# Performance work log

Hardware: AMD Instinct MI355X
Metric: run time of the kernel (lower is better)

## Reference

```python
import jax, jax.numpy as jnp
import numpy as np

H = 4        # num_heads
KNN = 10     # k_knn neighbors gathered by distance
KS = 4       # k_select top-k neighbors kept by attention score
EPS = 1e-5
BIG = 1e9


def _ln(x, g, b):
    m = x.mean(-1, keepdims=True)
    v = ((x - m) ** 2).mean(-1, keepdims=True)
    return (x - m) * jax.lax.rsqrt(v + EPS) * g + b


def _sparse_dyn_voxel_attn(x, coords, mask, w_qkv, b_qkv, w_proj, b_proj):
    # x: [B,N,C], coords: [B,N,3], mask: [B,N] bool
    B, N, C = x.shape
    dh = C // H
    qkv = x @ w_qkv + b_qkv                       # [B,N,3C]
    q, k, v = jnp.split(qkv, 3, axis=-1)
    q = q.reshape(B, N, H, dh).transpose(0, 2, 1, 3)   # [B,H,N,dh]
    k = k.reshape(B, N, H, dh).transpose(0, 2, 1, 3)
    v = v.reshape(B, N, H, dh).transpose(0, 2, 1, 3)

    # KNN over voxel coordinates; empty voxels pushed to far distance
    d2 = jnp.sum((coords[:, :, None, :] - coords[:, None, :, :]) ** 2, axis=-1)  # [B,N,N]
    d2 = jnp.where(mask[:, None, :], d2, BIG)
    _, nbr = jax.lax.top_k(-d2, KNN)              # [B,N,KNN] nearest-neighbor indices

    # gather neighbor keys/values: [B,H,N,KNN,dh]
    kn = jax.vmap(lambda a, i: a[:, i, :])(k, nbr)
    vn = jax.vmap(lambda a, i: a[:, i, :])(v, nbr)
    nmask = jax.vmap(lambda m, i: m[i])(mask, nbr)  # [B,N,KNN]

    scale = float(1.0 / np.sqrt(dh))
    scores = jnp.einsum('bhnd,bhnkd->bhnk', q, kn) * scale  # [B,H,N,KNN]
    scores = scores + jnp.where(nmask, 0.0, -BIG)[:, None, :, :]

    # dynamic selection: keep top k_select neighbors by score, softmax over them
    sv, si = jax.lax.top_k(scores, KS)            # [B,H,N,KS]
    w = jax.nn.softmax(sv, axis=-1)
    vsel = jnp.take_along_axis(vn, si[..., None], axis=3)   # [B,H,N,KS,dh]
    o = jnp.einsum('bhnk,bhnkd->bhnd', w, vsel)   # [B,H,N,dh]
    o = o.transpose(0, 2, 1, 3).reshape(B, N, C) @ w_proj + b_proj
    return jnp.where(mask[..., None], o, 0.0)


def setup_inputs() -> dict:
    key = jax.random.key(0)
    ks = jax.random.split(key, 8)
    B, N, C, M = 4, 4096, 64, 256  # N = 16^3 voxels
    s = lambda k, sh: jax.random.normal(k, sh, jnp.float32) * 0.02
    return dict(
        inputs=jax.random.normal(ks[0], (B, N, C), jnp.float32),
        voxel_coords=jax.random.uniform(ks[1], (B, N, 3), jnp.float32) * 16.0,
        non_empty_mask=jax.random.randint(ks[2], (B, N), 0, 2).astype(bool),
        ln1_g=jnp.ones(C, jnp.float32), ln1_b=jnp.zeros(C, jnp.float32),
        ln2_g=jnp.ones(C, jnp.float32), ln2_b=jnp.zeros(C, jnp.float32),
        w_qkv=s(ks[3], (C, 3 * C)), b_qkv=jnp.zeros(3 * C, jnp.float32),
        w_proj=s(ks[4], (C, C)), b_proj=jnp.zeros(C, jnp.float32),
        w1=s(ks[5], (C, M)), b1=jnp.zeros(M, jnp.float32),
        w2=s(ks[6], (M, C)), b2=jnp.zeros(C, jnp.float32),
    )


def reference(inputs, voxel_coords, non_empty_mask, ln1_g, ln1_b, ln2_g, ln2_b,
              w_qkv, b_qkv, w_proj, b_proj, w1, b1, w2, b2):
    a = _sparse_dyn_voxel_attn(_ln(inputs, ln1_g, ln1_b), voxel_coords,
                               non_empty_mask, w_qkv, b_qkv, w_proj, b_proj)
    x = 0.5 * a + inputs                          # drop_path(attn)*0.5 + shortcut (eval)
    h = jax.nn.gelu(_ln(x, ln2_g, ln2_b) @ w1 + b1) @ w2 + b2
    return 0.5 * h + x
```

## Files before the change

### kernel.cpp

```cpp
#include <hip/hip_runtime.h>
#include <hip/hip_bf16.h>
#include <math.h>

#define NH   4
#define DH   16
#define CH   64
#define KNN  10
#define KS   4
#define NV   4096
#define NB   4
#define MHID 256
#define BN   (NB * NV)

#define P_LN1G  0
#define P_LN1B  64
#define P_LN2G  128
#define P_LN2B  192
#define P_WQKV  256
#define P_BQKV  12544
#define P_WPROJ 12736
#define P_BPROJ 16832
#define P_W1    16896
#define P_B1    33280
#define P_W2    33536
#define P_B2    49920
#define P_TOT   49984

#define N_ING  (BN * CH + NB * NV * 3 + P_TOT + BN)
#define N_PACK (16384 + 16384 + 12288)

typedef __hip_bfloat16 bf16;
typedef __attribute__((ext_vector_type(8))) short short8;
typedef __attribute__((ext_vector_type(4))) float float4a;

__device__ __forceinline__ float b2f(bf16 x) { return __bfloat162float(x); }

__device__ __forceinline__ float cvt(const void* p, int i, int isbf) {
  return isbf ? b2f(((const bf16*)p)[i]) : ((const float*)p)[i];
}

__device__ __forceinline__ float wave_sum_f32(float v) {
#pragma unroll
  for (int m = 32; m >= 1; m >>= 1) v += __shfl_xor(v, m, 64);
  return v;
}

__device__ __forceinline__ int wave_sum_i32(int v) {
#pragma unroll
  for (int m = 32; m >= 1; m >>= 1) v += __shfl_xor(v, m, 64);
  return v;
}

__device__ __forceinline__ void wave_min_kv(unsigned& hi, unsigned& lo) {
#pragma unroll
  for (int m = 32; m >= 1; m >>= 1) {
    unsigned ohi = __shfl_xor(hi, m, 64);
    unsigned olo = __shfl_xor(lo, m, 64);
    if (ohi < hi || (ohi == hi && olo < lo)) { hi = ohi; lo = olo; }
  }
}

__device__ __forceinline__ float tanh_fast(float u) {
  float e = __expf(2.0f * u);
  return 1.0f - 2.0f / (e + 1.0f);
}

__device__ __forceinline__ float d2f(float x, float y, float z,
                                     float qx, float qy, float qz) {
  float dx = x - qx, dy = y - qy, dz = z - qz;
  return dx * dx + dy * dy + dz * dz;
}

__device__ __forceinline__ void knn_insert(unsigned long long* arr,
                                           unsigned long long key) {
  if (key < arr[KNN - 1]) {
#pragma unroll
    for (int t = 0; t < KNN; ++t) {
      unsigned long long a = arr[t];
      bool lt = key < a;
      unsigned long long mn = lt ? key : a;
      unsigned long long mx = lt ? a : key;
      arr[t] = mn;
      key = mx;
    }
  }
}

__global__ __launch_bounds__(256) void k_prep(
    const void* xin, const void* coords, const void* maskr,
    const void* ln1g, const void* ln1b, const void* ln2g, const void* ln2b,
    const void* wqkv, const void* bqkv, const void* wproj, const void* bproj,
    const void* w1, const void* b1, const void* w2, const void* b2,
    float* __restrict__ xcan, float* __restrict__ ccan,
    float* __restrict__ pcan, int* __restrict__ mcan,
    unsigned short* __restrict__ w1p, unsigned short* __restrict__ w2p,
    unsigned short* __restrict__ wqp, int* __restrict__ flags)
{
  __shared__ int sfl[2];
  const int tid = threadIdx.x;
  if (tid < 64) {
    const unsigned short* xu = (const unsigned short*)xin;
    const unsigned* mu = (const unsigned*)maskr;
    int cnt = 0;
#pragma unroll
    for (int k = 0; k < 4; ++k) {
      unsigned short w = xu[tid * 4 + k];
      int e = (w >> 7) & 0xFF;
      cnt += (e >= 100 && e <= 140);
    }
#pragma unroll
    for (int m = 32; m >= 1; m >>= 1) cnt += __shfl_xor(cnt, m, 64);
    unsigned big = (mu[tid] > 1u) ? 1u : 0u;
#pragma unroll
    for (int m = 32; m >= 1; m >>= 1) big |= __shfl_xor(big, m, 64);
    if (tid == 0) {
      sfl[0] = (cnt >= 205) ? 1 : 0;
      sfl[1] = big ? 1 : 0;
      if (blockIdx.x == 0) { flags[0] = sfl[0]; flags[1] = sfl[1]; }
    }
  }
  __syncthreads();
  const int isbf = sfl[0], m8 = sfl[1];

  int id = blockIdx.x * 256 + tid;
  const int n0 = BN * CH, n1 = NB * NV * 3, n2 = P_TOT, n3 = BN;
  if (id < n0) { xcan[id] = cvt(xin, id, isbf); return; }
  id -= n0;
  if (id < n1) { ccan[id] = cvt(coords, id, isbf); return; }
  id -= n1;
  if (id < n2) {
    const void* src; int off;
    if      (id < P_LN1B)  { src = ln1g;  off = id - P_LN1G; }
    else if (id < P_LN2G)  { src = ln1b;  off = id - P_LN1B; }
    else if (id < P_LN2B)  { src = ln2g;  off = id - P_LN2G; }
    else if (id < P_WQKV)  { src = ln2b;  off = id - P_LN2B; }
    else if (id < P_BQKV)  { src = wqkv;  off = id - P_WQKV; }
    else if (id < P_WPROJ) { src = bqkv;  off = id - P_BQKV; }
    else if (id < P_BPROJ) { src = wproj; off = id - P_WPROJ; }
    else if (id < P_W1)    { src = bproj; off = id - P_BPROJ; }
    else if (id < P_B1)    { src = w1;    off = id - P_W1; }
    else if (id < P_W2)    { src = b1;    off = id - P_B1; }
    else if (id < P_B2)    { src = w2;    off = id - P_W2; }
    else                   { src = b2;    off = id - P_B2; }
    pcan[id] = cvt(src, off, isbf);
    return;
  }
  id -= n2;
  if (id < n3) {
    mcan[id] = m8 ? (int)(((const unsigned char*)maskr)[id] != 0)
                  : (int)(((const int*)maskr)[id] != 0);
    return;
  }
  id -= n3;
  if (id < 16384) {
    int j = id & 7, l = (id >> 3) & 63, kh = (id >> 9) & 1, nt = id >> 10;
    int k = kh * 32 + ((l >> 4) * 8) + j;
    int n = nt * 16 + (l & 15);
    w1p[id] = __bfloat16_as_ushort(__float2bfloat16(cvt(w1, k * MHID + n, isbf)));
    return;
  }
  id -= 16384;
  if (id < 16384) {
    int j = id & 7, l = (id >> 3) & 63, kh = (id >> 9) & 7, nt = id >> 12;
    int k = kh * 32 + ((l >> 4) * 8) + j;
    int n = nt * 16 + (l & 15);
    w2p[id] = __bfloat16_as_ushort(__float2bfloat16(cvt(w2, k * CH + n, isbf)));
    return;
  }
  id -= 16384;
  if (id < 12288) {
    int j = id & 7, l = (id >> 3) & 63, kh = (id >> 9) & 1, nt = id >> 10;
    int k = kh * 32 + ((l >> 4) * 8) + j;
    int n = nt * 16 + (l & 15);
    wqp[id] = __bfloat16_as_ushort(__float2bfloat16(cvt(wqkv, k * 192 + n, isbf)));
  }
}

#define XQS 72
__global__ __launch_bounds__(256) void k_ln_qkv(
    const float* __restrict__ x, const float* __restrict__ pcan,
    const unsigned short* __restrict__ wqp, float* __restrict__ qkv)
{
  __shared__ unsigned short xnb[16 * XQS];
  const int tid = threadIdx.x;
  const int wave = tid >> 6, lane = tid & 63;
  const int row0 = blockIdx.x * 16;

  {
    const float gg = pcan[P_LN1G + lane], bb = pcan[P_LN1B + lane];
#pragma unroll
    for (int r = 0; r < 4; ++r) {
      int m = wave * 4 + r;
      float v = x[(size_t)(row0 + m) * CH + lane];
      float mn = wave_sum_f32(v) * (1.0f / 64.0f);
      float d = v - mn;
      float var = wave_sum_f32(d * d) * (1.0f / 64.0f);
      float rs = 1.0f / sqrtf(var + 1e-5f);
      xnb[m * XQS + lane] =
          __bfloat16_as_ushort(__float2bfloat16(d * rs * gg + bb));
    }
  }
  __syncthreads();

  const int q = lane >> 4, c = lane & 15;
  short8 a0 = *(const short8*)&xnb[c * XQS + q * 8];
  short8 a1 = *(const short8*)&xnb[c * XQS + 32 + q * 8];

#pragma unroll
  for (int t = 0; t < 3; ++t) {
    int nt = wave * 3 + t;
    short8 b0 = *(const short8*)&wqp[(size_t)((nt * 2 + 0) * 64 + lane) * 8];
    short8 b1 = *(const short8*)&wqp[(size_t)((nt * 2 + 1) * 64 + lane) * 8];
    float4a z = {0.f, 0.f, 0.f, 0.f};
    z = __builtin_amdgcn_mfma_f32_16x16x32_bf16(a0, b0, z, 0, 0, 0);
    z = __builtin_amdgcn_mfma_f32_16x16x32_bf16(a1, b1, z, 0, 0, 0);
    int n = nt * 16 + c;
    float bq = pcan[P_BQKV + n];
#pragma unroll
    for (int r = 0; r < 4; ++r) {
      int m = q * 4 + r;
      qkv[(size_t)(row0 + m) * 192 + n] = z[r] + bq;
    }
  }
}

__global__ __launch_bounds__(1024) void k_bin(
    const float* __restrict__ ccan, const int* __restrict__ mcan,
    float4* __restrict__ pbin, unsigned* __restrict__ bstart)
{
  __shared__ unsigned cnt[NV];
  __shared__ unsigned woff[16];
  const int b = blockIdx.x, tid = threadIdx.x;
  const float* cb = ccan + (size_t)b * NV * 3;
  const int* mb = mcan + b * NV;
  unsigned* st = bstart + (size_t)b * 4104;

#pragma unroll
  for (int k = 0; k < 4; ++k) cnt[tid + k * 1024] = 0;
  __syncthreads();

#pragma unroll
  for (int k = 0; k < 4; ++k) {
    int j = tid + k * 1024;
    if (mb[j]) {
      int cx = (int)cb[j * 3];     cx = cx > 15 ? 15 : cx;
      int cy = (int)cb[j * 3 + 1]; cy = cy > 15 ? 15 : cy;
      int cz = (int)cb[j * 3 + 2]; cz = cz > 15 ? 15 : cz;
      atomicAdd(&cnt[(cz << 8) + (cy << 4) + cx], 1u);
    }
  }
  __syncthreads();

  unsigned s0 = cnt[tid * 4], s1 = cnt[tid * 4 + 1];
  unsigned s2 = cnt[tid * 4 + 2], s3 = cnt[tid * 4 + 3];
  unsigned tot = s0 + s1 + s2 + s3;
  unsigned v = tot;
  const int wv = tid >> 6, ln = tid & 63;
#pragma unroll
  for (int d = 1; d < 64; d <<= 1) {
    unsigned o = __shfl_up(v, d, 64);
    if (ln >= d) v += o;
  }
  if (ln == 63) woff[wv] = v;
  __syncthreads();
  unsigned wpre = 0;
  for (int w = 0; w < wv; ++w) wpre += woff[w];
  unsigned r = wpre + v - tot;
  cnt[tid * 4]     = r; st[tid * 4]     = r; r += s0;
  cnt[tid * 4 + 1] = r; st[tid * 4 + 1] = r; r += s1;
  cnt[tid * 4 + 2] = r; st[tid * 4 + 2] = r; r += s2;
  cnt[tid * 4 + 3] = r; st[tid * 4 + 3] = r; r += s3;
  if (tid == 1023) st[4096] = r;
  __syncthreads();

#pragma unroll
  for (int k = 0; k < 4; ++k) {
    int j = tid + k * 1024;
    if (mb[j]) {
      float x = cb[j * 3], y = cb[j * 3 + 1], z = cb[j * 3 + 2];
      int cx = (int)x; cx = cx > 15 ? 15 : cx;
      int cy = (int)y; cy = cy > 15 ? 15 : cy;
      int cz = (int)z; cz = cz > 15 ? 15 : cz;
      unsigned pos = atomicAdd(&cnt[(cz << 8) + (cy << 4) + cx], 1u);
      float4 q; q.x = x; q.y = y; q.z = z; q.w = __int_as_float(j);
      pbin[(size_t)b * NV + pos] = q;
    }
  }
}

__global__ __launch_bounds__(256) void k_knn4(
    const float4* __restrict__ pbin, const unsigned* __restrict__ bstart,
    int* __restrict__ nbr)
{
  const int wave = threadIdx.x >> 6, lane = threadIdx.x & 63;
  const int b = blockIdx.x >> 10;
  const int slot = (blockIdx.x & 1023) * 4 + wave;
  const unsigned* st = bstart + (size_t)b * 4104;
  const int nval = (int)st[4096];
  if (slot >= nval) return;
  const float4* gpt = pbin + (size_t)b * NV;

  const float4 me = gpt[slot];
  const float qx = me.x, qy = me.y, qz = me.z;
  const int qi = __float_as_int(me.w);
  int cz = (int)qz; cz = cz > 15 ? 15 : cz;

  unsigned long long arr[KNN];
#pragma unroll
  for (int t = 0; t < KNN; ++t) arr[t] = ~0ull;

  int R = 2;
  int zlo = cz - 2 < 0 ? 0 : cz - 2;
  int zhi = cz + 2 > 15 ? 15 : cz + 2;
  {
    const int s = (int)st[zlo << 8], e = (int)st[(zhi + 1) << 8];
    for (int i = s + lane; i < e; i += 64) {
      float4 p = gpt[i];
      float d2 = d2f(p.x, p.y, p.z, qx, qy, qz);
      knn_insert(arr, ((unsigned long long)__float_as_uint(d2) << 32) |
                      (unsigned)__float_as_int(p.w));
    }
  }

  for (;;) {
    const float RR = (float)(R * R);
    int c = 0;
#pragma unroll
    for (int t = 0; t < KNN; ++t) {
      float d = __uint_as_float((unsigned)(arr[t] >> 32));
      c += (d <= RR) ? 1 : 0;
    }
    c = wave_sum_i32(c);
    if (c >= KNN) break;
    if (zlo == 0 && zhi == 15) break;
    ++R;
    const int nzlo = cz - R < 0 ? 0 : cz - R;
    const int nzhi = cz + R > 15 ? 15 : cz + R;
    {
      const int s = (int)st[nzlo << 8], e = (int)st[zlo << 8];
      for (int i = s + lane; i < e; i += 64) {
        float4 p = gpt[i];
        float d2 = d2f(p.x, p.y, p.z, qx, qy, qz);
        knn_insert(arr, ((unsigned long long)__float_as_uint(d2) << 32) |
                        (unsigned)__float_as_int(p.w));
      }
    }
    {
      const int s = (int)st[(zhi + 1) << 8], e = (int)st[(nzhi + 1) << 8];
      for (int i = s + lane; i < e; i += 64) {
        float4 p = gpt[i];
        float d2 = d2f(p.x, p.y, p.z, qx, qy, qz);
        knn_insert(arr, ((unsigned long long)__float_as_uint(d2) << 32) |
                        (unsigned)__float_as_int(p.w));
      }
    }
    zlo = nzlo; zhi = nzhi;
  }

  unsigned myj = 0;
#pragma unroll 1
  for (int r = 0; r < KNN; ++r) {
    unsigned hi = (unsigned)(arr[0] >> 32);
    unsigned lo = (unsigned)(arr[0] & 0xffffffffu);
    wave_min_kv(hi, lo);
    const unsigned long long win = ((unsigned long long)hi << 32) | lo;
    if (arr[0] == win) {
#pragma unroll
      for (int t = 0; t < KNN - 1; ++t) arr[t] = arr[t + 1];
      arr[KNN - 1] = ~0ull;
    }
    if (lane == r) myj = lo;
  }
  const int row = (b << 12) | qi;
  if (lane < KNN) nbr[(size_t)row * KNN + lane] = (int)(myj & (NV - 1));
}

#define AROWS 4
__global__ __launch_bounds__(256) void k_attn(
    const float* __restrict__ qkv, const int* __restrict__ nbr,
    const int* __restrict__ mcan, const float* __restrict__ xcan,
    const float* __restrict__ pcan, float* __restrict__ xres)
{
  __shared__ float wp[CH * CH];
  __shared__ float bp[CH];
  __shared__ float sc[AROWS][NH][KNN];
  __shared__ float wsel[AROWS][NH][KS];
  __shared__ int   isel[AROWS][NH][KS];
  __shared__ float obuf[AROWS][CH];
  __shared__ int   nb[AROWS][KNN];
  __shared__ float npen[AROWS][KNN];
  const int tid = threadIdx.x;
  {
    const float4* src = (const float4*)(pcan + P_WPROJ);
    float4* dst = (float4*)wp;
    for (int i = tid; i < CH * CH / 4; i += 256) dst[i] = src[i];
    if (tid < CH) bp[tid] = pcan[P_BPROJ + tid];
  }
  const int wave = tid >> 6, lane = tid & 63;
  const int row = blockIdx.x * AROWS + wave;
  const int b = row / NV;
  const bool live = mcan[row] != 0;

  if (live && lane < KNN) {
    int j = nbr[(size_t)row * KNN + lane] & (NV - 1);
    nb[wave][lane] = j;
    npen[wave][lane] = mcan[b * NV + j] ? 0.0f : -1e9f;
  }
  __syncthreads();

  if (live && lane < NH * KNN) {
    int h = lane / KNN, kk = lane % KNN;
    int j = nb[wave][kk];
    const float* qp = qkv + (size_t)row * 192 + h * DH;
    const float* kp = qkv + ((size_t)(b * NV + j)) * 192 + 64 + h * DH;
    float acc = 0.f;
#pragma unroll
    for (int d = 0; d < DH; ++d) acc += qp[d] * kp[d];
    sc[wave][h][kk] = acc * 0.25f + npen[wave][kk];
  }
  __syncthreads();

  if (live && lane < NH) {
    int h = lane;
    float sv[KS]; int sj[KS];
    unsigned used = 0;
#pragma unroll
    for (int r = 0; r < KS; ++r) {
      float best = -INFINITY; int bi = 0;
#pragma unroll
      for (int kk = 0; kk < KNN; ++kk) {
        float s = sc[wave][h][kk];
        if (!(used & (1u << kk)) && s > best) { best = s; bi = kk; }
      }
      used |= 1u << bi; sv[r] = best; sj[r] = bi;
    }
    float mx = sv[0];
    float e[KS], sum = 0.f;
#pragma unroll
    for (int r = 0; r < KS; ++r) { e[r] = expf(sv[r] - mx); sum += e[r]; }
    float inv = 1.0f / sum;
#pragma unroll
    for (int r = 0; r < KS; ++r) {
      wsel[wave][h][r] = e[r] * inv;
      isel[wave][h][r] = nb[wave][sj[r]];
    }
  }
  __syncthreads();

  if (live) {
    int h = lane >> 4, d = lane & 15;
    float o = 0.f;
#pragma unroll
    for (int r = 0; r < KS; ++r) {
      int j = isel[wave][h][r];
      o += wsel[wave][h][r] * qkv[((size_t)(b * NV + j)) * 192 + 128 + h * DH + d];
    }
    obuf[wave][lane] = o;
  }
  __syncthreads();

  if (live) {
    float acc = bp[lane];
#pragma unroll 4
    for (int cc = 0; cc < CH; ++cc)
      acc = fmaf(obuf[wave][cc], wp[cc * CH + lane], acc);
    xres[(size_t)row * CH + lane] = 0.5f * acc + xcan[(size_t)row * CH + lane];
  } else {
    xres[(size_t)row * CH + lane] = xcan[(size_t)row * CH + lane];
  }
}

#define XNS 72
#define GS  264
__global__ __launch_bounds__(256) void k_mlp(
    const float* __restrict__ xres, const float* __restrict__ pcan,
    const unsigned short* __restrict__ w1p,
    const unsigned short* __restrict__ w2p,
    const int* __restrict__ flags, void* __restrict__ out)
{
  __shared__ unsigned short xnb[16 * XNS];
  __shared__ unsigned short gb[16 * GS];
  const int tid = threadIdx.x;
  const int wave = tid >> 6, lane = tid & 63;
  const int row0 = blockIdx.x * 16;

  {
    const float gg = pcan[P_LN2G + lane], bb2 = pcan[P_LN2B + lane];
#pragma unroll
    for (int r = 0; r < 4; ++r) {
      int m = wave * 4 + r;
      float v = xres[(size_t)(row0 + m) * CH + lane];
      float mn = wave_sum_f32(v) * (1.0f / 64.0f);
      float d = v - mn;
      float var = wave_sum_f32(d * d) * (1.0f / 64.0f);
      float rs = 1.0f / sqrtf(var + 1e-5f);
      xnb[m * XNS + lane] =
          __bfloat16_as_ushort(__float2bfloat16(d * rs * gg + bb2));
    }
  }
  __syncthreads();

  const int q = lane >> 4, c = lane & 15;
  short8 a0 = *(const short8*)&xnb[c * XNS + q * 8];
  short8 a1 = *(const short8*)&xnb[c * XNS + 32 + q * 8];

  float4a acc[4];
#pragma unroll
  for (int t = 0; t < 4; ++t) {
    int nt = wave * 4 + t;
    short8 b0 = *(const short8*)&w1p[(size_t)((nt * 2 + 0) * 64 + lane) * 8];
    short8 b1 = *(const short8*)&w1p[(size_t)((nt * 2 + 1) * 64 + lane) * 8];
    float4a z = {0.f, 0.f, 0.f, 0.f};
    z = __builtin_amdgcn_mfma_f32_16x16x32_bf16(a0, b0, z, 0, 0, 0);
    z = __builtin_amdgcn_mfma_f32_16x16x32_bf16(a1, b1, z, 0, 0, 0);
    acc[t] = z;
  }
#pragma unroll
  for (int t = 0; t < 4; ++t) {
    int n = (wave * 4 + t) * 16 + c;
    float bo = pcan[P_B1 + n];
#pragma unroll
    for (int r = 0; r < 4; ++r) {
      float h = acc[t][r] + bo;
      float u = 0.7978845608028654f * (h + 0.044715f * h * h * h);
      float gv = 0.5f * h * (1.0f + tanh_fast(u));
      gb[(q * 4 + r) * GS + n] = __bfloat16_as_ushort(__float2bfloat16(gv));
    }
  }
  __syncthreads();

  float4a o = {0.f, 0.f, 0.f, 0.f};
#pragma unroll
  for (int kh = 0; kh < 8; ++kh) {
    short8 ag = *(const short8*)&gb[c * GS + kh * 32 + q * 8];
    short8 bg = *(const short8*)&w2p[(size_t)((wave * 8 + kh) * 64 + lane) * 8];
    o = __builtin_amdgcn_mfma_f32_16x16x32_bf16(ag, bg, o, 0, 0, 0);
  }
  {
    int n = wave * 16 + c;
    float b2v = pcan[P_B2 + n];
    const int isbf = flags[0];
#pragma unroll
    for (int r = 0; r < 4; ++r) {
      int m = q * 4 + r;
      size_t idx = (size_t)(row0 + m) * CH + n;
      float val = 0.5f * (o[r] + b2v) + xres[idx];
      if (isbf) ((bf16*)out)[idx] = __float2bfloat16(val);
      else      ((float*)out)[idx] = val;
    }
  }
}

extern "C" void kernel_launch(void* const* d_in, const int* in_sizes, int n_in,
                              void* d_out, int out_size, void* d_ws, size_t ws_size,
                              hipStream_t stream)
{
  char* ws = (char*)d_ws;
  float* qkv   = (float*)(ws);
  float* xres  = (float*)(ws + 12582912);
  float* xcan  = (float*)(ws + 16777216);
  float* ccan  = (float*)(ws + 20971520);
  float* pcan  = (float*)(ws + 21168128);
  int*   mcan  = (int*)  (ws + 21368064);
  int*   nbr   = (int*)  (ws + 21433600);
  int*   flags = (int*)  (ws + 22088960);
  unsigned short* w1p = (unsigned short*)(ws + 22089728);
  unsigned short* w2p = (unsigned short*)(ws + 22122496);
  unsigned short* wqp = (unsigned short*)(ws + 22155264);
  float4*   pbin   = (float4*)  (ws + 22179840);
  unsigned* bstart = (unsigned*)(ws + 22441984);

  const int total = N_ING + N_PACK;
  k_prep<<<(total + 255) / 256, 256, 0, stream>>>(
      d_in[0], d_in[1], d_in[2], d_in[3], d_in[4], d_in[5], d_in[6],
      d_in[7], d_in[8], d_in[9], d_in[10], d_in[11], d_in[12], d_in[13], d_in[14],
      xcan, ccan, pcan, mcan, w1p, w2p, wqp, flags);
  k_bin<<<NB, 1024, 0, stream>>>(ccan, mcan, pbin, bstart);
  k_ln_qkv<<<BN / 16, 256, 0, stream>>>(xcan, pcan, wqp, qkv);
  k_knn4<<<NB * (NV / 4), 256, 0, stream>>>(pbin, bstart, nbr);
  k_attn<<<BN / AROWS, 256, 0, stream>>>(qkv, nbr, mcan, xcan, pcan, xres);
  k_mlp<<<BN / 16, 256, 0, stream>>>(xres, pcan, w1p, w2p, flags, d_out);
}
```

Baseline: 156.3 us.

## Fuse attention and MLP kernels and vectorize input canonicalization

```diff
diff --git a/kernel.cpp b/kernel.cpp
--- a/kernel.cpp
+++ b/kernel.cpp
@@ -27,6 +27,7 @@
 #define P_TOT   49984
 
 #define N_ING  (BN * CH + NB * NV * 3 + P_TOT + BN)
+#define N_ING4 (N_ING / 4)
 #define N_PACK (16384 + 16384 + 12288)
 
 typedef __hip_bfloat16 bf16;
@@ -37,6 +38,21 @@
 
 __device__ __forceinline__ float cvt(const void* p, int i, int isbf) {
   return isbf ? b2f(((const bf16*)p)[i]) : ((const float*)p)[i];
+}
+
+__device__ __forceinline__ float us2f(unsigned short u) {
+  return __uint_as_float(((unsigned)u) << 16);
+}
+
+__device__ __forceinline__ float4 cvt4(const void* p, int i, int isbf) {
+  float4 r;
+  if (isbf) {
+    ushort4 u = *(const ushort4*)((const unsigned short*)p + i);
+    r.x = us2f(u.x); r.y = us2f(u.y); r.z = us2f(u.z); r.w = us2f(u.w);
+  } else {
+    r = *(const float4*)((const float*)p + i);
+  }
+  return r;
 }
 
 __device__ __forceinline__ float wave_sum_f32(float v) {
@@ -123,35 +139,43 @@
   const int isbf = sfl[0], m8 = sfl[1];
 
   int id = blockIdx.x * 256 + tid;
-  const int n0 = BN * CH, n1 = NB * NV * 3, n2 = P_TOT, n3 = BN;
-  if (id < n0) { xcan[id] = cvt(xin, id, isbf); return; }
-  id -= n0;
-  if (id < n1) { ccan[id] = cvt(coords, id, isbf); return; }
-  id -= n1;
-  if (id < n2) {
-    const void* src; int off;
-    if      (id < P_LN1B)  { src = ln1g;  off = id - P_LN1G; }
-    else if (id < P_LN2G)  { src = ln1b;  off = id - P_LN1B; }
-    else if (id < P_LN2B)  { src = ln2g;  off = id - P_LN2G; }
-    else if (id < P_WQKV)  { src = ln2b;  off = id - P_LN2B; }
-    else if (id < P_BQKV)  { src = wqkv;  off = id - P_WQKV; }
-    else if (id < P_WPROJ) { src = bqkv;  off = id - P_BQKV; }
-    else if (id < P_BPROJ) { src = wproj; off = id - P_WPROJ; }
-    else if (id < P_W1)    { src = bproj; off = id - P_BPROJ; }
-    else if (id < P_B1)    { src = w1;    off = id - P_W1; }
-    else if (id < P_W2)    { src = b1;    off = id - P_B1; }
-    else if (id < P_B2)    { src = w2;    off = id - P_W2; }
-    else                   { src = b2;    off = id - P_B2; }
-    pcan[id] = cvt(src, off, isbf);
+  if (id < N_ING4) {
+    int e4 = id * 4;
+    const int n0 = BN * CH, n1 = NB * NV * 3, n2 = P_TOT;
+    if (e4 < n0) { *(float4*)&xcan[e4] = cvt4(xin, e4, isbf); return; }
+    e4 -= n0;
+    if (e4 < n1) { *(float4*)&ccan[e4] = cvt4(coords, e4, isbf); return; }
+    e4 -= n1;
+    if (e4 < n2) {
+      const void* src; int off;
+      if      (e4 < P_LN1B)  { src = ln1g;  off = e4 - P_LN1G; }
+      else if (e4 < P_LN2G)  { src = ln1b;  off = e4 - P_LN1B; }
+      else if (e4 < P_LN2B)  { src = ln2g;  off = e4 - P_LN2G; }
+      else if (e4 < P_WQKV)  { src = ln2b;  off = e4 - P_LN2B; }
+      else if (e4 < P_BQKV)  { src = wqkv;  off = e4 - P_WQKV; }
+      else if (e4 < P_WPROJ) { src = bqkv;  off = e4 - P_BQKV; }
+      else if (e4 < P_BPROJ) { src = wproj; off = e4 - P_WPROJ; }
+      else if (e4 < P_W1)    { src = bproj; off = e4 - P_BPROJ; }
+      else if (e4 < P_B1)    { src = w1;    off = e4 - P_W1; }
+      else if (e4 < P_W2)    { src = b1;    off = e4 - P_B1; }
+      else if (e4 < P_B2)    { src = w2;    off = e4 - P_W2; }
+      else                   { src = b2;    off = e4 - P_B2; }
+      *(float4*)&pcan[e4] = cvt4(src, off, isbf);
+      return;
+    }
+    e4 -= n2;
+    if (m8) {
+      uchar4 u = *(const uchar4*)((const unsigned char*)maskr + e4);
+      mcan[e4 + 0] = u.x != 0; mcan[e4 + 1] = u.y != 0;
+      mcan[e4 + 2] = u.z != 0; mcan[e4 + 3] = u.w != 0;
+    } else {
+      int4 v = *(const int4*)((const int*)maskr + e4);
+      mcan[e4 + 0] = v.x != 0; mcan[e4 + 1] = v.y != 0;
+      mcan[e4 + 2] = v.z != 0; mcan[e4 + 3] = v.w != 0;
+    }
     return;
   }
-  id -= n2;
-  if (id < n3) {
-    mcan[id] = m8 ? (int)(((const unsigned char*)maskr)[id] != 0)
-                  : (int)(((const int*)maskr)[id] != 0);
-    return;
-  }
-  id -= n3;
+  id -= N_ING4;
   if (id < 16384) {
     int j = id & 7, l = (id >> 3) & 63, kh = (id >> 9) & 1, nt = id >> 10;
     int k = kh * 32 + ((l >> 4) * 8) + j;
@@ -375,121 +399,124 @@
   if (lane < KNN) nbr[(size_t)row * KNN + lane] = (int)(myj & (NV - 1));
 }
 
-#define AROWS 4
-__global__ __launch_bounds__(256) void k_attn(
+#define XNS 72
+#define GS  264
+__global__ __launch_bounds__(256) void k_attn_mlp(
     const float* __restrict__ qkv, const int* __restrict__ nbr,
     const int* __restrict__ mcan, const float* __restrict__ xcan,
-    const float* __restrict__ pcan, float* __restrict__ xres)
+    const float* __restrict__ pcan,
+    const unsigned short* __restrict__ w1p,
+    const unsigned short* __restrict__ w2p,
+    const int* __restrict__ flags, void* __restrict__ out)
 {
   __shared__ float wp[CH * CH];
   __shared__ float bp[CH];
-  __shared__ float sc[AROWS][NH][KNN];
-  __shared__ float wsel[AROWS][NH][KS];
-  __shared__ int   isel[AROWS][NH][KS];
-  __shared__ float obuf[AROWS][CH];
-  __shared__ int   nb[AROWS][KNN];
-  __shared__ float npen[AROWS][KNN];
+  __shared__ float otile[16][CH];
+  __shared__ float xtile[16][CH];
+  __shared__ float sc[4][NH][KNN];
+  __shared__ float wsel[4][NH][KS];
+  __shared__ int   isel[4][NH][KS];
+  __shared__ int   nb[4][KNN];
+  __shared__ float npen[4][KNN];
+  __shared__ unsigned short xnb[16 * XNS];
+  __shared__ unsigned short gb[16 * GS];
   const int tid = threadIdx.x;
+  const int wave = tid >> 6, lane = tid & 63;
+  const int row0 = blockIdx.x * 16;
+  const int b = row0 / NV;
+
   {
     const float4* src = (const float4*)(pcan + P_WPROJ);
     float4* dst = (float4*)wp;
     for (int i = tid; i < CH * CH / 4; i += 256) dst[i] = src[i];
     if (tid < CH) bp[tid] = pcan[P_BPROJ + tid];
   }
-  const int wave = tid >> 6, lane = tid & 63;
-  const int row = blockIdx.x * AROWS + wave;
-  const int b = row / NV;
-  const bool live = mcan[row] != 0;
-
-  if (live && lane < KNN) {
-    int j = nbr[(size_t)row * KNN + lane] & (NV - 1);
-    nb[wave][lane] = j;
-    npen[wave][lane] = mcan[b * NV + j] ? 0.0f : -1e9f;
-  }
-  __syncthreads();
-
-  if (live && lane < NH * KNN) {
-    int h = lane / KNN, kk = lane % KNN;
-    int j = nb[wave][kk];
-    const float* qp = qkv + (size_t)row * 192 + h * DH;
-    const float* kp = qkv + ((size_t)(b * NV + j)) * 192 + 64 + h * DH;
-    float acc = 0.f;
-#pragma unroll
-    for (int d = 0; d < DH; ++d) acc += qp[d] * kp[d];
-    sc[wave][h][kk] = acc * 0.25f + npen[wave][kk];
-  }
-  __syncthreads();
-
-  if (live && lane < NH) {
-    int h = lane;
-    float sv[KS]; int sj[KS];
-    unsigned used = 0;
-#pragma unroll
-    for (int r = 0; r < KS; ++r) {
-      float best = -INFINITY; int bi = 0;
-#pragma unroll
-      for (int kk = 0; kk < KNN; ++kk) {
-        float s = sc[wave][h][kk];
-        if (!(used & (1u << kk)) && s > best) { best = s; bi = kk; }
+  __syncthreads();
+
+#pragma unroll 1
+  for (int r = 0; r < 4; ++r) {
+    const int m = wave * 4 + r;
+    const int row = row0 + m;
+    if (mcan[row]) {
+      if (lane < KNN) {
+        int j = nbr[(size_t)row * KNN + lane] & (NV - 1);
+        nb[wave][lane] = j;
+        npen[wave][lane] = mcan[b * NV + j] ? 0.0f : -1e9f;
       }
-      used |= 1u << bi; sv[r] = best; sj[r] = bi;
-    }
-    float mx = sv[0];
-    float e[KS], sum = 0.f;
-#pragma unroll
-    for (int r = 0; r < KS; ++r) { e[r] = expf(sv[r] - mx); sum += e[r]; }
-    float inv = 1.0f / sum;
-#pragma unroll
-    for (int r = 0; r < KS; ++r) {
-      wsel[wave][h][r] = e[r] * inv;
-      isel[wave][h][r] = nb[wave][sj[r]];
-    }
-  }
-  __syncthreads();
-
-  if (live) {
-    int h = lane >> 4, d = lane & 15;
-    float o = 0.f;
-#pragma unroll
-    for (int r = 0; r < KS; ++r) {
-      int j = isel[wave][h][r];
-      o += wsel[wave][h][r] * qkv[((size_t)(b * NV + j)) * 192 + 128 + h * DH + d];
-    }
-    obuf[wave][lane] = o;
-  }
-  __syncthreads();
-
-  if (live) {
-    float acc = bp[lane];
+      __builtin_amdgcn_wave_barrier();
+      if (lane < NH * KNN) {
+        int h = lane / KNN, kk = lane % KNN;
+        int j = nb[wave][kk];
+        const float* qp = qkv + (size_t)row * 192 + h * DH;
+        const float* kp = qkv + ((size_t)(b * NV + j)) * 192 + 64 + h * DH;
+        float acc = 0.f;
+#pragma unroll
+        for (int d = 0; d < DH; ++d) acc += qp[d] * kp[d];
+        sc[wave][h][kk] = acc * 0.25f + npen[wave][kk];
+      }
+      __builtin_amdgcn_wave_barrier();
+      if (lane < NH) {
+        int h = lane;
+        float sv[KS]; int sj[KS];
+        unsigned used = 0;
+#pragma unroll
+        for (int rr = 0; rr < KS; ++rr) {
+          float best = -INFINITY; int bi = 0;
+#pragma unroll
+          for (int kk = 0; kk < KNN; ++kk) {
+            float s = sc[wave][h][kk];
+            if (!(used & (1u << kk)) && s > best) { best = s; bi = kk; }
+          }
+          used |= 1u << bi; sv[rr] = best; sj[rr] = bi;
+        }
+        float mx = sv[0];
+        float e[KS], sum = 0.f;
+#pragma unroll
+        for (int rr = 0; rr < KS; ++rr) { e[rr] = expf(sv[rr] - mx); sum += e[rr]; }
+        float inv = 1.0f / sum;
+#pragma unroll
+        for (int rr = 0; rr < KS; ++rr) {
+          wsel[wave][h][rr] = e[rr] * inv;
+          isel[wave][h][rr] = nb[wave][sj[rr]];
+        }
+      }
+      __builtin_amdgcn_wave_barrier();
+      {
+        int h = lane >> 4, d = lane & 15;
+        float o = 0.f;
+#pragma unroll
+        for (int rr = 0; rr < KS; ++rr) {
+          int j = isel[wave][h][rr];
+          o += wsel[wave][h][rr] *
+               qkv[((size_t)(b * NV + j)) * 192 + 128 + h * DH + d];
+        }
+        otile[m][lane] = o;
+      }
+      __builtin_amdgcn_wave_barrier();
+    }
+  }
+
+#pragma unroll 1
+  for (int r = 0; r < 4; ++r) {
+    const int m = wave * 4 + r;
+    const int row = row0 + m;
+    float x = xcan[(size_t)row * CH + lane];
+    if (mcan[row]) {
+      float acc = bp[lane];
 #pragma unroll 4
-    for (int cc = 0; cc < CH; ++cc)
-      acc = fmaf(obuf[wave][cc], wp[cc * CH + lane], acc);
-    xres[(size_t)row * CH + lane] = 0.5f * acc + xcan[(size_t)row * CH + lane];
-  } else {
-    xres[(size_t)row * CH + lane] = xcan[(size_t)row * CH + lane];
-  }
-}
-
-#define XNS 72
-#define GS  264
-__global__ __launch_bounds__(256) void k_mlp(
-    const float* __restrict__ xres, const float* __restrict__ pcan,
-    const unsigned short* __restrict__ w1p,
-    const unsigned short* __restrict__ w2p,
-    const int* __restrict__ flags, void* __restrict__ out)
-{
-  __shared__ unsigned short xnb[16 * XNS];
-  __shared__ unsigned short gb[16 * GS];
-  const int tid = threadIdx.x;
-  const int wave = tid >> 6, lane = tid & 63;
-  const int row0 = blockIdx.x * 16;
+      for (int cc = 0; cc < CH; ++cc)
+        acc = fmaf(otile[m][cc], wp[cc * CH + lane], acc);
+      x += 0.5f * acc;
+    }
+    xtile[m][lane] = x;
+  }
 
   {
     const float gg = pcan[P_LN2G + lane], bb2 = pcan[P_LN2B + lane];
 #pragma unroll
     for (int r = 0; r < 4; ++r) {
       int m = wave * 4 + r;
-      float v = xres[(size_t)(row0 + m) * CH + lane];
+      float v = xtile[m][lane];
       float mn = wave_sum_f32(v) * (1.0f / 64.0f);
       float d = v - mn;
       float var = wave_sum_f32(d * d) * (1.0f / 64.0f);
@@ -504,7 +531,7 @@
   short8 a0 = *(const short8*)&xnb[c * XNS + q * 8];
   short8 a1 = *(const short8*)&xnb[c * XNS + 32 + q * 8];
 
-  float4a acc[4];
+  float4a acc1[4];
 #pragma unroll
   for (int t = 0; t < 4; ++t) {
     int nt = wave * 4 + t;
@@ -513,7 +540,7 @@
     float4a z = {0.f, 0.f, 0.f, 0.f};
     z = __builtin_amdgcn_mfma_f32_16x16x32_bf16(a0, b0, z, 0, 0, 0);
     z = __builtin_amdgcn_mfma_f32_16x16x32_bf16(a1, b1, z, 0, 0, 0);
-    acc[t] = z;
+    acc1[t] = z;
   }
 #pragma unroll
   for (int t = 0; t < 4; ++t) {
@@ -521,7 +548,7 @@
     float bo = pcan[P_B1 + n];
 #pragma unroll
     for (int r = 0; r < 4; ++r) {
-      float h = acc[t][r] + bo;
+      float h = acc1[t][r] + bo;
       float u = 0.7978845608028654f * (h + 0.044715f * h * h * h);
       float gv = 0.5f * h * (1.0f + tanh_fast(u));
       gb[(q * 4 + r) * GS + n] = __bfloat16_as_ushort(__float2bfloat16(gv));
@@ -544,7 +571,7 @@
     for (int r = 0; r < 4; ++r) {
       int m = q * 4 + r;
       size_t idx = (size_t)(row0 + m) * CH + n;
-      float val = 0.5f * (o[r] + b2v) + xres[idx];
+      float val = 0.5f * (o[r] + b2v) + xtile[m][n];
       if (isbf) ((bf16*)out)[idx] = __float2bfloat16(val);
       else      ((float*)out)[idx] = val;
     }
@@ -557,7 +584,6 @@
 {
   char* ws = (char*)d_ws;
   float* qkv   = (float*)(ws);
-  float* xres  = (float*)(ws + 12582912);
   float* xcan  = (float*)(ws + 16777216);
   float* ccan  = (float*)(ws + 20971520);
   float* pcan  = (float*)(ws + 21168128);
@@ -570,7 +596,7 @@
   float4*   pbin   = (float4*)  (ws + 22179840);
   unsigned* bstart = (unsigned*)(ws + 22441984);
 
-  const int total = N_ING + N_PACK;
+  const int total = N_ING4 + N_PACK;
   k_prep<<<(total + 255) / 256, 256, 0, stream>>>(
       d_in[0], d_in[1], d_in[2], d_in[3], d_in[4], d_in[5], d_in[6],
       d_in[7], d_in[8], d_in[9], d_in[10], d_in[11], d_in[12], d_in[13], d_in[14],
@@ -578,6 +604,6 @@
   k_bin<<<NB, 1024, 0, stream>>>(ccan, mcan, pbin, bstart);
   k_ln_qkv<<<BN / 16, 256, 0, stream>>>(xcan, pcan, wqp, qkv);
   k_knn4<<<NB * (NV / 4), 256, 0, stream>>>(pbin, bstart, nbr);
-  k_attn<<<BN / AROWS, 256, 0, stream>>>(qkv, nbr, mcan, xcan, pcan, xres);
-  k_mlp<<<BN / 16, 256, 0, stream>>>(xres, pcan, w1p, w2p, flags, d_out);
-}
+  k_attn_mlp<<<BN / 16, 256, 0, stream>>>(qkv, nbr, mcan, xcan, pcan,
+                                          w1p, w2p, flags, d_out);
+}
```

New measurement: 150.7 us. 3.6% less time.
